# Performance work log

Hardware: AMD Instinct MI355X
Metric: run time of the kernel (lower is better)

The kernel has to match this reference:

```python
import jax, jax.numpy as jnp
import numpy as np
from functools import partial


def setup_inputs() -> dict:
    key = jax.random.key(0)
    ks = jax.random.split(key, 8)
    B, D, H, K, T = 256, 2048, 2048, 64, 32
    s = 1.0 / np.sqrt(H)  # PyTorch-style uniform init scale (use normal*s for simplicity)
    return {
        "x": jax.random.normal(ks[0], (B, D), dtype=jnp.float32),
        "eps": jax.random.normal(ks[1], (T, B, K), dtype=jnp.float32),
        "W_ih": jax.random.normal(ks[2], (4 * H, D), dtype=jnp.float32) * s,
        "W_hh": jax.random.normal(ks[3], (4 * H, H), dtype=jnp.float32) * s,
        "b_ih": jax.random.normal(ks[4], (4 * H,), dtype=jnp.float32) * s,
        "b_hh": jax.random.normal(ks[5], (4 * H,), dtype=jnp.float32) * s,
        "W_fe": jax.random.normal(ks[6], (2 * K, H), dtype=jnp.float32) * s,
        "b_fe": jax.random.normal(ks[7], (2 * K,), dtype=jnp.float32) * s,
        "num_ticks": T,
    }


def reference(x, eps, W_ih, W_hh, b_ih, b_hh, W_fe, b_fe, num_ticks):
    B = x.shape[0]
    H = W_hh.shape[1]
    K = eps.shape[-1]
    # x is fed unchanged every tick, so its gate contribution is precomputable.
    xg = x @ W_ih.T + b_ih + b_hh  # [B, 4H]

    def step(carry, e):
        h, c = carry
        g = xg + h @ W_hh.T  # [B, 4H]
        i, f, gg, o = jnp.split(g, 4, axis=-1)  # PyTorch LSTMCell gate order: i, f, g, o
        i = jax.nn.sigmoid(i)
        f = jax.nn.sigmoid(f)
        gg = jnp.tanh(gg)
        o = jax.nn.sigmoid(o)
        c = f * c + i * gg
        h = o * jnp.tanh(c)
        fe = h @ W_fe.T + b_fe  # [B, 2K]
        mus = fe[:, :K]
        sig = jax.nn.softplus(fe[:, K:] - 5.0)
        z = e * sig + mus
        return (h, c), (z, mus, sig)

    h0 = jnp.zeros((B, H), dtype=x.dtype)
    c0 = jnp.zeros((B, H), dtype=x.dtype)
    (h, c), (zs, mus, sigs) = jax.lax.scan(step, (h0, c0), eps)
    # torch stacks along dim=-1 -> [B, K, T]
    zs = jnp.moveaxis(zs, 0, -1)
    mus = jnp.moveaxis(mus, 0, -1)
    sigs = jnp.moveaxis(sigs, 0, -1)
    return zs, mus, sigs, (h, c)
```

## Files before the change

kernel.cpp:

```cpp
#include <hip/hip_runtime.h>
#include <math.h>


typedef short  short8  __attribute__((ext_vector_type(8)));
typedef float  floatx4 __attribute__((ext_vector_type(4)));

#define BB 256
#define HH 2048
#define G4 8192
#define KK 64
#define TT 32

__device__ __forceinline__ unsigned short f2bf(float f) {
  union { float f; unsigned int u; } v; v.f = f;
  unsigned int u = v.u;
  u += 0x7fffu + ((u >> 16) & 1u);
  return (unsigned short)(u >> 16);
}
__device__ __forceinline__ float sigmoidf_(float x) { return 1.0f / (1.0f + __expf(-x)); }
__device__ __forceinline__ float softplusf_(float x) {
  return (x > 20.0f) ? x : log1pf(__expf(x));
}
__device__ __forceinline__ short8 cvt8(const float* __restrict__ s) {
  float4 a = reinterpret_cast<const float4*>(s)[0];
  float4 b = reinterpret_cast<const float4*>(s)[1];
  short8 o;
  o[0] = f2bf(a.x); o[1] = f2bf(a.y); o[2] = f2bf(a.z); o[3] = f2bf(a.w);
  o[4] = f2bf(b.x); o[5] = f2bf(b.y); o[6] = f2bf(b.z); o[7] = f2bf(b.w);
  return o;
}

template <int PERM>
__global__ void cvt_w_kernel(const float* __restrict__ in,
                             unsigned short* __restrict__ out, int total) {
  int tid = blockIdx.x * 256 + threadIdx.x;
  if (tid >= total) return;
  int col = tid & 31;
  int k4  = (tid >> 5) & 63;
  int ph  = (tid >> 11) & 1;
  int blk = tid >> 12;
  int q = blk * 32 + col;
  int srcrow = PERM ? ((q & 3) * HH + (q >> 2)) : q;
  const float* src = in + (size_t)srcrow * HH + (ph * 128 + k4 * 2) * 8;
  short8 o0 = cvt8(src);
  short8 o1 = cvt8(src + 8);
  size_t ch = ((size_t)(blk * 2 + ph) * 128 + k4 * 2) * 32 + col;
  reinterpret_cast<short8*>(out)[ch]      = o0;
  reinterpret_cast<short8*>(out)[ch + 32] = o1;
}

__global__ void cvt_x_kernel(const float* __restrict__ in,
                             unsigned short* __restrict__ out) {
  int tid = blockIdx.x * 256 + threadIdx.x;
  int row = tid & 255, k8 = tid >> 8;
  short8 o = cvt8(in + (size_t)row * HH + k8 * 8);
  reinterpret_cast<short8*>(out)[tid] = o;
}

__device__ __forceinline__ void core_gemm(const short8* __restrict__ A8,
                                          const short8* __restrict__ Wg8,
                                          short8* L8, floatx4 acc[2][2]) {
  const int tid = threadIdx.x;
  const int lane = tid & 63, wave = tid >> 6;
  const int l15 = lane & 15, l4 = lane >> 4;
  const short8* Lr = L8 + l4 * 32 + l15;
  const int abase = l4 * 256 + wave * 32 + l15;
  for (int ph = 0; ph < 2; ++ph) {
    __syncthreads();
#pragma unroll
    for (int j = 0; j < 8; ++j)
      L8[tid + j * 512] = Wg8[ph * 4096 + tid + j * 512];
    __syncthreads();
    short8 Ar[4][2];
#pragma unroll
    for (int i = 0; i < 4; ++i) {
      Ar[i][0] = A8[abase +      (ph * 128 + i * 4) * 256];
      Ar[i][1] = A8[abase + 16 + (ph * 128 + i * 4) * 256];
    }
#pragma unroll
    for (int kt = 0; kt < 32; ++kt) {
      short8 a0 = Ar[kt & 3][0], a1 = Ar[kt & 3][1];
      if (kt < 28) {
        Ar[kt & 3][0] = A8[abase +      (ph * 128 + (kt + 4) * 4) * 256];
        Ar[kt & 3][1] = A8[abase + 16 + (ph * 128 + (kt + 4) * 4) * 256];
      }
      short8 b0 = Lr[kt * 128];
      short8 b1 = Lr[kt * 128 + 16];
      acc[0][0] = __builtin_amdgcn_mfma_f32_16x16x32_bf16(a0, b0, acc[0][0], 0, 0, 0);
      acc[0][1] = __builtin_amdgcn_mfma_f32_16x16x32_bf16(a0, b1, acc[0][1], 0, 0, 0);
      acc[1][0] = __builtin_amdgcn_mfma_f32_16x16x32_bf16(a1, b0, acc[1][0], 0, 0, 0);
      acc[1][1] = __builtin_amdgcn_mfma_f32_16x16x32_bf16(a1, b1, acc[1][1], 0, 0, 0);
    }
  }
}

__global__ __launch_bounds__(1024) void lstm_loop_kernel(
    unsigned short* __restrict__ HallT, const unsigned short* __restrict__ Wt2,
    const float* __restrict__ xg, float* __restrict__ outh,
    float* __restrict__ outc, unsigned int* __restrict__ bar) {
  __shared__ __align__(16) unsigned short Wlds[65536];
  const int tid = threadIdx.x;
  const int lane = tid & 63, wave = tid >> 6;
  const int l15 = lane & 15, l4 = lane >> 4;
  const int qb = blockIdx.x * 32, rw = wave * 16;
  const int gate = l15 & 3;
  const int base = lane & ~3;

  float xgr[2][4];
#pragma unroll
  for (int ct = 0; ct < 2; ++ct) {
    const int q = qb + ct * 16 + l15;
#pragma unroll
    for (int r = 0; r < 4; ++r) {
      const int row = rw + l4 * 4 + r;
      xgr[ct][r] = xg[(size_t)row * G4 + q];
    }
  }

  short8* L8 = reinterpret_cast<short8*>(Wlds);
  {
    const short8* Wg8 = reinterpret_cast<const short8*>(Wt2)
                        + (size_t)blockIdx.x * 8192;
#pragma unroll
    for (int j = 0; j < 8; ++j)
      L8[tid + j * 1024] = Wg8[tid + j * 1024];
  }
  __syncthreads();

  const short8* Lr = L8 + l4 * 32 + l15;
  const int abase = l4 * 256 + wave * 16 + l15;

  float creg[2][4];
#pragma unroll
  for (int ct = 0; ct < 2; ++ct)
#pragma unroll
    for (int r = 0; r < 4; ++r) creg[ct][r] = 0.0f;

#pragma unroll 1
  for (int t = 0; t < TT; ++t) {
    unsigned short* Hout = HallT + (size_t)(t + 1) * 524288;

    floatx4 acc[2];
    floatx4 z4 = {0.f, 0.f, 0.f, 0.f};
    acc[0] = z4; acc[1] = z4;

    if (t > 0) {
      const short8* Ap = reinterpret_cast<const short8*>(HallT)
                         + (size_t)t * 65536 + abase;
      short8 Ar[8];
#pragma unroll
      for (int i = 0; i < 8; ++i) Ar[i] = Ap[i * 1024];
#pragma unroll
      for (int kt = 0; kt < 64; ++kt) {
        short8 a0 = Ar[kt & 7];
        if (kt < 56) Ar[kt & 7] = Ap[(kt + 8) * 1024];
        short8 b0 = Lr[kt * 128];
        short8 b1 = Lr[kt * 128 + 16];
        acc[0] = __builtin_amdgcn_mfma_f32_16x16x32_bf16(a0, b0, acc[0], 0, 0, 0);
        acc[1] = __builtin_amdgcn_mfma_f32_16x16x32_bf16(a0, b1, acc[1], 0, 0, 0);
      }
    }

    const int last = (t == TT - 1);
#pragma unroll
    for (int ct = 0; ct < 2; ++ct) {
      const floatx4 av = acc[ct];
      const int q = qb + ct * 16 + l15;
      const int u = q >> 2;
#pragma unroll
      for (int r = 0; r < 4; ++r) {
        const int row = rw + l4 * 4 + r;
        float g = av[r] + xgr[ct][r];
        float act = (gate == 2) ? tanhf(g) : sigmoidf_(g);
        float iv = __shfl(act, base);
        float fv = __shfl(act, base + 1);
        float gv = __shfl(act, base + 2);
        float ov = __shfl(act, base + 3);
        if (gate == 0) {
          float cnew = fv * creg[ct][r] + iv * gv;
          float hnew = ov * tanhf(cnew);
          creg[ct][r] = cnew;
          Hout[(size_t)(blockIdx.x * 256 + row) * 8 + (u & 7)] = f2bf(hnew);
          if (last) {
            const size_t ci = (size_t)row * HH + u;
            outh[ci] = hnew; outc[ci] = cnew;
          }
        }
      }
    }

    if (t < TT - 1) {
      __syncthreads();
      if (tid == 0) {
        __hip_atomic_fetch_add(bar, 1u, __ATOMIC_RELEASE,
                               __HIP_MEMORY_SCOPE_AGENT);
        const unsigned int target = (unsigned int)(t + 1) * 256u;
        while (__hip_atomic_load(bar, __ATOMIC_ACQUIRE,
                                 __HIP_MEMORY_SCOPE_AGENT) < target)
          __builtin_amdgcn_s_sleep(2);
      }
      __syncthreads();
    }
  }
}

__global__ __launch_bounds__(512) void xg_kernel(
    const unsigned short* __restrict__ XT, const unsigned short* __restrict__ Wih,
    const float* __restrict__ b_ih, const float* __restrict__ b_hh,
    float* __restrict__ xg) {
  __shared__ __align__(16) unsigned short Wlds[32768];
  floatx4 acc[2][2];
  floatx4 z4 = {0.f, 0.f, 0.f, 0.f};
  acc[0][0] = z4; acc[0][1] = z4; acc[1][0] = z4; acc[1][1] = z4;
  core_gemm(reinterpret_cast<const short8*>(XT),
            reinterpret_cast<const short8*>(Wih) + (size_t)blockIdx.x * 8192,
            reinterpret_cast<short8*>(Wlds), acc);

  const int tid = threadIdx.x, lane = tid & 63, wave = tid >> 6;
  const int l15 = lane & 15, l4 = lane >> 4;
  const int qb = blockIdx.x * 32, rw = wave * 32;
#pragma unroll
  for (int rt = 0; rt < 2; ++rt)
#pragma unroll
    for (int ct = 0; ct < 2; ++ct) {
      const int q = qb + ct * 16 + l15;
      const float bias = b_ih[(q & 3) * HH + (q >> 2)] + b_hh[(q & 3) * HH + (q >> 2)];
#pragma unroll
      for (int r = 0; r < 4; ++r) {
        const int row = rw + rt * 16 + l4 * 4 + r;
        xg[(size_t)row * G4 + q] = acc[rt][ct][r] + bias;
      }
    }
}

__global__ __launch_bounds__(512) void fe_kernel(
    const unsigned short* __restrict__ HallT, const unsigned short* __restrict__ Wfe,
    const float* __restrict__ b_fe, float* __restrict__ fe) {
  const int t = blockIdx.x >> 2, cg_ = blockIdx.x & 3;
  __shared__ __align__(16) unsigned short Wlds[32768];
  floatx4 acc[2][2];
  floatx4 z4 = {0.f, 0.f, 0.f, 0.f};
  acc[0][0] = z4; acc[0][1] = z4; acc[1][0] = z4; acc[1][1] = z4;
  core_gemm(reinterpret_cast<const short8*>(HallT) + (size_t)(t + 1) * 65536,
            reinterpret_cast<const short8*>(Wfe) + (size_t)cg_ * 8192,
            reinterpret_cast<short8*>(Wlds), acc);

  const int tid = threadIdx.x, lane = tid & 63, wave = tid >> 6;
  const int l15 = lane & 15, l4 = lane >> 4;
  const int rw = wave * 32;
#pragma unroll
  for (int rt = 0; rt < 2; ++rt)
#pragma unroll
    for (int ct = 0; ct < 2; ++ct) {
      const int col = cg_ * 32 + ct * 16 + l15;
      const float bias = b_fe[col];
#pragma unroll
      for (int r = 0; r < 4; ++r) {
        const int row = rw + rt * 16 + l4 * 4 + r;
        fe[((size_t)t * 256 + row) * 128 + col] = acc[rt][ct][r] + bias;
      }
    }
}

__global__ void z_kernel(const float* __restrict__ eps, const float* __restrict__ fe,
                         float* __restrict__ out) {
  const int tid = blockIdx.x * blockDim.x + threadIdx.x;
  const int tt = tid >> 14;
  const int b = (tid >> 6) & 255;
  const int k = tid & 63;
  const int frow = tt * 256 + b;
  const float mus = fe[frow * 128 + k];
  const float sig = softplusf_(fe[frow * 128 + 64 + k] - 5.0f);
  const float z = eps[tid] * sig + mus;
  const int o = (b * KK + k) * TT + tt;
  out[o] = z;
  out[524288 + o] = mus;
  out[2 * 524288 + o] = sig;
}

extern "C" void kernel_launch(void* const* d_in, const int* in_sizes, int n_in,
                              void* d_out, int out_size, void* d_ws, size_t ws_size,
                              hipStream_t stream) {
  const float* x    = (const float*)d_in[0];
  const float* eps  = (const float*)d_in[1];
  const float* W_ih = (const float*)d_in[2];
  const float* W_hh = (const float*)d_in[3];
  const float* b_ih = (const float*)d_in[4];
  const float* b_hh = (const float*)d_in[5];
  const float* W_fe = (const float*)d_in[6];
  const float* b_fe = (const float*)d_in[7];
  float* out = (float*)d_out;

  const size_t BH  = (size_t)BB * HH;
  const size_t BKT = (size_t)BB * KK * TT;

  char* p = (char*)d_ws;
  auto nxt = [&](size_t bytes) -> char* {
    char* r = p; p += (bytes + 255) & ~(size_t)255; return r;
  };
  unsigned short* Wbig  = (unsigned short*)nxt((size_t)G4 * HH * 2);
  float*          xg    = (float*)nxt((size_t)BB * G4 * 4);
  unsigned short* HallT = (unsigned short*)nxt((size_t)(TT + 1) * BH * 2);
  unsigned short* XT    = (unsigned short*)nxt(BH * 2);
  unsigned short* Wfeb  = (unsigned short*)nxt((size_t)128 * HH * 2);
  float*          fe    = (float*)nxt((size_t)(TT * BB) * 128 * 4);
  unsigned int*   bar   = (unsigned int*)nxt(256);

  hipMemsetAsync(bar, 0, 256, stream);

  cvt_x_kernel<<<256, 256, 0, stream>>>(x, XT);
  cvt_w_kernel<0><<<64, 256, 0, stream>>>(W_fe, Wfeb, 16384);
  cvt_w_kernel<1><<<4096, 256, 0, stream>>>(W_ih, Wbig, 1048576);
  xg_kernel<<<256, 512, 0, stream>>>(XT, Wbig, b_ih, b_hh, xg);
  cvt_w_kernel<1><<<4096, 256, 0, stream>>>(W_hh, Wbig, 1048576);

  lstm_loop_kernel<<<256, 1024, 0, stream>>>(
      HallT, Wbig, xg, out + 3 * BKT, out + 3 * BKT + BH, bar);

  fe_kernel<<<128, 512, 0, stream>>>(HallT, Wfeb, b_fe, fe);
  z_kernel<<<2048, 256, 0, stream>>>(eps, fe, out);
}
```

Baseline: 1.045 ms.

## Use 32x32x16 MFMA with split-K across waves and LDS reduction in LSTM loop

The recurrent matmul in the persistent LSTM kernel moves from 16x16x32 MFMA tiles to 32x32x16 tiles. Each wave now covers a 32-row by 32-gate tile over half of K, and the two K halves are summed through a new shared-memory buffer. This halves the LDS weight reads per MFMA and raises arithmetic intensity per wave. In exchange it adds an extra block-wide barrier and LDS round trip each step, and only half the waves run the gate nonlinearities.

```diff
diff --git a/kernel.cpp b/kernel.cpp
--- a/kernel.cpp
+++ b/kernel.cpp
@@ -2,8 +2,9 @@
 #include <math.h>
 
 
-typedef short  short8  __attribute__((ext_vector_type(8)));
-typedef float  floatx4 __attribute__((ext_vector_type(4)));
+typedef short  short8   __attribute__((ext_vector_type(8)));
+typedef float  floatx4  __attribute__((ext_vector_type(4)));
+typedef float  floatx16 __attribute__((ext_vector_type(16)));
 
 #define BB 256
 #define HH 2048
@@ -99,23 +100,23 @@
     const float* __restrict__ xg, float* __restrict__ outh,
     float* __restrict__ outc, unsigned int* __restrict__ bar) {
   __shared__ __align__(16) unsigned short Wlds[65536];
+  __shared__ __align__(16) float Rlds[8192];
   const int tid = threadIdx.x;
   const int lane = tid & 63, wave = tid >> 6;
-  const int l15 = lane & 15, l4 = lane >> 4;
-  const int qb = blockIdx.x * 32, rw = wave * 16;
-  const int gate = l15 & 3;
+  const int rt = wave & 7, kh = wave >> 3;
+  const int l31 = lane & 31, l5 = lane >> 5;
+  const int qb = blockIdx.x * 32;
+  const int gate = lane & 3;
   const int base = lane & ~3;
 
-  float xgr[2][4];
-#pragma unroll
-  for (int ct = 0; ct < 2; ++ct) {
-    const int q = qb + ct * 16 + l15;
+  float xgr[4][4];
+#pragma unroll
+  for (int q4 = 0; q4 < 4; ++q4)
 #pragma unroll
     for (int r = 0; r < 4; ++r) {
-      const int row = rw + l4 * 4 + r;
-      xgr[ct][r] = xg[(size_t)row * G4 + q];
-    }
-  }
+      const int row = rt * 32 + r + 8 * q4 + 4 * l5;
+      xgr[q4][r] = xg[(size_t)row * G4 + qb + l31];
+    }
 
   short8* L8 = reinterpret_cast<short8*>(Wlds);
   {
@@ -127,66 +128,86 @@
   }
   __syncthreads();
 
-  const short8* Lr = L8 + l4 * 32 + l15;
-  const int abase = l4 * 256 + wave * 16 + l15;
-
-  float creg[2][4];
-#pragma unroll
-  for (int ct = 0; ct < 2; ++ct)
-#pragma unroll
-    for (int r = 0; r < 4; ++r) creg[ct][r] = 0.0f;
+  const short8* Lb = L8 + kh * 4096 + lane;
+  const int abase = (kh * 128 + l5) * 256 + rt * 32 + l31;
+
+  float creg[4][4];
+#pragma unroll
+  for (int q4 = 0; q4 < 4; ++q4)
+#pragma unroll
+    for (int r = 0; r < 4; ++r) creg[q4][r] = 0.0f;
+
+  float4* R4 = reinterpret_cast<float4*>(Rlds);
 
 #pragma unroll 1
   for (int t = 0; t < TT; ++t) {
     unsigned short* Hout = HallT + (size_t)(t + 1) * 524288;
 
-    floatx4 acc[2];
-    floatx4 z4 = {0.f, 0.f, 0.f, 0.f};
-    acc[0] = z4; acc[1] = z4;
+    floatx16 acc = {0.f, 0.f, 0.f, 0.f, 0.f, 0.f, 0.f, 0.f,
+                    0.f, 0.f, 0.f, 0.f, 0.f, 0.f, 0.f, 0.f};
 
     if (t > 0) {
       const short8* Ap = reinterpret_cast<const short8*>(HallT)
                          + (size_t)t * 65536 + abase;
       short8 Ar[8];
 #pragma unroll
-      for (int i = 0; i < 8; ++i) Ar[i] = Ap[i * 1024];
-#pragma unroll
-      for (int kt = 0; kt < 64; ++kt) {
-        short8 a0 = Ar[kt & 7];
-        if (kt < 56) Ar[kt & 7] = Ap[(kt + 8) * 1024];
-        short8 b0 = Lr[kt * 128];
-        short8 b1 = Lr[kt * 128 + 16];
-        acc[0] = __builtin_amdgcn_mfma_f32_16x16x32_bf16(a0, b0, acc[0], 0, 0, 0);
-        acc[1] = __builtin_amdgcn_mfma_f32_16x16x32_bf16(a0, b1, acc[1], 0, 0, 0);
-      }
-    }
-
-    const int last = (t == TT - 1);
-#pragma unroll
-    for (int ct = 0; ct < 2; ++ct) {
-      const floatx4 av = acc[ct];
-      const int q = qb + ct * 16 + l15;
-      const int u = q >> 2;
-#pragma unroll
-      for (int r = 0; r < 4; ++r) {
-        const int row = rw + l4 * 4 + r;
-        float g = av[r] + xgr[ct][r];
-        float act = (gate == 2) ? tanhf(g) : sigmoidf_(g);
-        float iv = __shfl(act, base);
-        float fv = __shfl(act, base + 1);
-        float gv = __shfl(act, base + 2);
-        float ov = __shfl(act, base + 3);
-        if (gate == 0) {
-          float cnew = fv * creg[ct][r] + iv * gv;
-          float hnew = ov * tanhf(cnew);
-          creg[ct][r] = cnew;
-          Hout[(size_t)(blockIdx.x * 256 + row) * 8 + (u & 7)] = f2bf(hnew);
-          if (last) {
-            const size_t ci = (size_t)row * HH + u;
-            outh[ci] = hnew; outc[ci] = cnew;
+      for (int i = 0; i < 8; ++i) Ar[i] = Ap[i * 512];
+      short8 Brg[2];
+      Brg[0] = Lb[0];
+#pragma unroll
+      for (int step = 0; step < 64; ++step) {
+        short8 a = Ar[step & 7];
+        short8 b = Brg[step & 1];
+        if (step < 63) Brg[(step + 1) & 1] = Lb[(step + 1) * 64];
+        if (step < 56) Ar[step & 7] = Ap[(step + 8) * 512];
+        acc = __builtin_amdgcn_mfma_f32_32x32x16_bf16(a, b, acc, 0, 0, 0);
+      }
+
+      if (kh == 1) {
+#pragma unroll
+        for (int q4 = 0; q4 < 4; ++q4) {
+          float4 v = {acc[4 * q4], acc[4 * q4 + 1], acc[4 * q4 + 2], acc[4 * q4 + 3]};
+          R4[rt * 256 + q4 * 64 + lane] = v;
+        }
+      }
+      __syncthreads();
+      if (kh == 0) {
+#pragma unroll
+        for (int q4 = 0; q4 < 4; ++q4) {
+          float4 v = R4[rt * 256 + q4 * 64 + lane];
+          acc[4 * q4]     += v.x;
+          acc[4 * q4 + 1] += v.y;
+          acc[4 * q4 + 2] += v.z;
+          acc[4 * q4 + 3] += v.w;
+        }
+      }
+    }
+
+    if (kh == 0) {
+      const int last = (t == TT - 1);
+      const int u7 = l31 >> 2;
+#pragma unroll
+      for (int q4 = 0; q4 < 4; ++q4)
+#pragma unroll
+        for (int r = 0; r < 4; ++r) {
+          const int row = rt * 32 + r + 8 * q4 + 4 * l5;
+          float g = acc[q4 * 4 + r] + xgr[q4][r];
+          float act = (gate == 2) ? tanhf(g) : sigmoidf_(g);
+          float iv = __shfl(act, base);
+          float fv = __shfl(act, base + 1);
+          float gv = __shfl(act, base + 2);
+          float ov = __shfl(act, base + 3);
+          if (gate == 0) {
+            float cnew = fv * creg[q4][r] + iv * gv;
+            float hnew = ov * tanhf(cnew);
+            creg[q4][r] = cnew;
+            Hout[(size_t)(blockIdx.x * 256 + row) * 8 + u7] = f2bf(hnew);
+            if (last) {
+              const size_t ci = (size_t)row * HH + blockIdx.x * 8 + u7;
+              outh[ci] = hnew; outc[ci] = cnew;
+            }
           }
         }
-      }
     }
 
     if (t < TT - 1) {
```

Result: slower. 1.270 ms (+21.6%).
